# Optimization experiments

Measured on AMD Instinct MI355X. Metric: run time of the kernel, lower is better.

The kernel has to match this reference:

```python
import jax, jax.numpy as jnp
import numpy as np

N_TOKENS = 16384
DIM = 2048
HIDDEN = 1408
N_EXPERTS = 8


def setup_inputs() -> dict:
    key = jax.random.key(0)
    k_x, k_w1, k_w2, k_w3 = jax.random.split(key, 4)
    x = jax.random.normal(k_x, (N_TOKENS, DIM), dtype=jnp.float32)
    # trunc_normal(std=0.02) approximated by scaled normal
    w1 = jax.random.normal(k_w1, (N_EXPERTS, HIDDEN, DIM), dtype=jnp.float32) * 0.02
    w2 = jax.random.normal(k_w2, (N_EXPERTS, DIM, HIDDEN), dtype=jnp.float32) * 0.02
    w3 = jax.random.normal(k_w3, (N_EXPERTS, HIDDEN, DIM), dtype=jnp.float32) * 0.02
    # contiguous, even token split across experts (sums to N_TOKENS)
    num_tokens_per_expert = jnp.full((N_EXPERTS,), N_TOKENS // N_EXPERTS, dtype=jnp.int32)
    return {"x": x, "w1": w1, "w2": w2, "w3": w3,
            "num_tokens_per_expert": num_tokens_per_expert}


def reference(x, w1, w2, w3, num_tokens_per_expert):
    """Masked per-expert SwiGLU FFN (matches _run_experts_for_loop).

    x: [N, D] tokens sorted so expert e owns the contiguous slice
       [cumsum_shifted[e], cumsum[e]).
    """
    n_tokens = x.shape[0]
    n_experts = w1.shape[0]
    cumsum = jnp.cumsum(num_tokens_per_expert.astype(jnp.int32))
    cumsum_shifted = jnp.concatenate(
        [jnp.zeros((1,), dtype=cumsum.dtype), cumsum[:-1]])
    token_idx = jnp.arange(n_tokens)
    out = jnp.zeros_like(x)
    for e in range(n_experts):  # small fixed expert loop, unrolled under jit
        mask = ((token_idx >= cumsum_shifted[e]) & (token_idx < cumsum[e]))
        mask = mask.astype(x.dtype)[:, None]          # [N, 1]
        x_masked = x * mask                            # [N, D]
        h = jax.nn.silu(x_masked @ w1[e].T)            # [N, H]
        h = h * (x_masked @ w3[e].T)                   # [N, H]
        out = out + (h @ w2[e].T) * mask               # [N, D]
    return out
```

## Files before the change

### kernel.cpp

```cpp
#include <hip/hip_runtime.h>
#include <stdint.h>

#define NTOK 16384
#define DIM 2048
#define HIDDEN 1408
#define NEXP 8
#define NPRIME 2816

typedef short short8 __attribute__((ext_vector_type(8)));
typedef float f32x4 __attribute__((ext_vector_type(4)));
typedef unsigned short u16;

__device__ __forceinline__ u16 f2bf(float f) {
    uint32_t u = __float_as_uint(f);
    return (u16)((u + 0x7fffu + ((u >> 16) & 1u)) >> 16);
}

__device__ __forceinline__ void gload16(const u16* g, u16* l) {
    __builtin_amdgcn_global_load_lds(
        (const __attribute__((address_space(1))) void*)g,
        (__attribute__((address_space(3))) void*)l,
        16, 0, 0);
}

__global__ __launch_bounds__(256) void cvt_kernel(const float* __restrict__ src,
                                                  u16* __restrict__ dst, long n) {
    long i0 = ((long)blockIdx.x * 256 + threadIdx.x) * 8;
    long stride = (long)gridDim.x * 256 * 8;
    for (long i = i0; i < n; i += stride) {
        float4 a = *(const float4*)(src + i);
        float4 b = *(const float4*)(src + i + 4);
        uint4 o;
        o.x = (uint32_t)f2bf(a.x) | ((uint32_t)f2bf(a.y) << 16);
        o.y = (uint32_t)f2bf(a.z) | ((uint32_t)f2bf(a.w) << 16);
        o.z = (uint32_t)f2bf(b.x) | ((uint32_t)f2bf(b.y) << 16);
        o.w = (uint32_t)f2bf(b.z) | ((uint32_t)f2bf(b.w) << 16);
        *(uint4*)(dst + i) = o;
    }
}

__global__ __launch_bounds__(256) void cvt13_kernel(const float* __restrict__ w1,
                                                    const float* __restrict__ w3,
                                                    u16* __restrict__ dst) {
    const int r  = blockIdx.x;
    const int e  = r / NPRIME;
    const int np = r - e * NPRIME;
    const int p  = np >> 5;
    const int s  = (np >> 4) & 1;
    const int c  = np & 15;
    const int hcol = p * 16 + c;
    const float* src = (s ? w3 : w1) + ((size_t)e * HIDDEN + hcol) * DIM;
    u16* d = dst + (size_t)r * DIM;
    const int i = threadIdx.x * 8;
    float4 a = *(const float4*)(src + i);
    float4 b = *(const float4*)(src + i + 4);
    uint4 o;
    o.x = (uint32_t)f2bf(a.x) | ((uint32_t)f2bf(a.y) << 16);
    o.y = (uint32_t)f2bf(a.z) | ((uint32_t)f2bf(a.w) << 16);
    o.z = (uint32_t)f2bf(b.x) | ((uint32_t)f2bf(b.y) << 16);
    o.w = (uint32_t)f2bf(b.z) | ((uint32_t)f2bf(b.w) << 16);
    *(uint4*)(d + i) = o;
}

__global__ __launch_bounds__(256) void ffn1_kernel(
    const u16* __restrict__ xb, const u16* __restrict__ wb13,
    const int* __restrict__ ntpe, u16* __restrict__ hb)
{
    __shared__ u16 As[128 * 64];
    __shared__ u16 Bs[128 * 64];

    const int e  = blockIdx.z;
    const int mt = blockIdx.x;
    const int nt = blockIdx.y;

    int base = 0;
    #pragma unroll
    for (int i = 0; i < NEXP; ++i) base += (i < e) ? ntpe[i] : 0;
    const int cnt = ntpe[e];
    if (mt * 128 >= cnt) return;

    const int tid  = threadIdx.x;
    const int lane = tid & 63;
    const int wid  = tid >> 6;
    const int wr   = wid >> 1;
    const int wc   = wid & 1;
    const int lq   = lane >> 4;
    const int lm   = lane & 15;

    const size_t m0 = (size_t)base + (size_t)mt * 128;
    const u16* Ag = xb   + m0 * DIM;
    const u16* Bg = wb13 + ((size_t)e * NPRIME + nt * 128) * DIM;

    f32x4 acc[4][4] = {};

    for (int k0 = 0; k0 < DIM; k0 += 64) {
        if (k0) __syncthreads();
        #pragma unroll
        for (int it = 0; it < 4; ++it) {
            int c   = it * 256 + tid;
            int row = c >> 3;
            int col = ((c & 7) ^ (row & 7)) * 8;
            size_t go = (size_t)row * DIM + k0 + col;
            gload16(Ag + go, &As[c * 8]);
            gload16(Bg + go, &Bs[c * 8]);
        }
        __syncthreads();

        #pragma unroll
        for (int kk = 0; kk < 2; ++kk) {
            const int gc = kk * 4 + lq;
            short8 af[4], bf[4];
            #pragma unroll
            for (int i = 0; i < 4; ++i) {
                int ar = wr * 64 + i * 16 + lm;
                af[i] = *(const short8*)&As[ar * 64 + ((gc ^ (ar & 7)) << 3)];
                int br = wc * 64 + i * 16 + lm;
                bf[i] = *(const short8*)&Bs[br * 64 + ((gc ^ (br & 7)) << 3)];
            }
            #pragma unroll
            for (int i = 0; i < 4; ++i)
                #pragma unroll
                for (int j = 0; j < 4; ++j)
                    acc[i][j] = __builtin_amdgcn_mfma_f32_16x16x32_bf16(af[i], bf[j], acc[i][j], 0, 0, 0);
        }
    }

    #pragma unroll
    for (int i = 0; i < 4; ++i)
        #pragma unroll
        for (int jp = 0; jp < 4; jp += 2) {
            const int p = nt * 4 + wc * 2 + (jp >> 1);
            #pragma unroll
            for (int r = 0; r < 4; ++r) {
                int mrow = mt * 128 + wr * 64 + i * 16 + lq * 4 + r;
                if (mrow < cnt) {
                    float v1 = acc[i][jp][r];
                    float v3 = acc[i][jp + 1][r];
                    float h = (v1 / (1.f + __expf(-v1))) * v3;
                    hb[((size_t)base + mrow) * HIDDEN + p * 16 + lm] = f2bf(h);
                }
            }
        }
}

__global__ __launch_bounds__(256) void ffn2_kernel(
    const u16* __restrict__ hb, const u16* __restrict__ w2b,
    const int* __restrict__ ntpe, float* __restrict__ out)
{
    __shared__ u16 As[128 * 64];
    __shared__ u16 Bs[128 * 64];

    const int e  = blockIdx.z;
    const int mt = blockIdx.x;
    const int nt = blockIdx.y;

    int base = 0;
    #pragma unroll
    for (int i = 0; i < NEXP; ++i) base += (i < e) ? ntpe[i] : 0;
    const int cnt = ntpe[e];
    if (mt * 128 >= cnt) return;

    const int tid  = threadIdx.x;
    const int lane = tid & 63;
    const int wid  = tid >> 6;
    const int wr   = wid >> 1;
    const int wc   = wid & 1;
    const int lq   = lane >> 4;
    const int lm   = lane & 15;

    const size_t m0 = (size_t)base + (size_t)mt * 128;
    const int    n0 = nt * 128;
    const u16* Ag = hb  + m0 * HIDDEN;
    const u16* Bg = w2b + ((size_t)e * DIM + n0) * HIDDEN;

    f32x4 acc[4][4] = {};

    for (int k0 = 0; k0 < HIDDEN; k0 += 64) {
        if (k0) __syncthreads();
        #pragma unroll
        for (int it = 0; it < 4; ++it) {
            int c   = it * 256 + tid;
            int row = c >> 3;
            int col = ((c & 7) ^ (row & 7)) * 8;
            size_t go = (size_t)row * HIDDEN + k0 + col;
            gload16(Ag + go, &As[c * 8]);
            gload16(Bg + go, &Bs[c * 8]);
        }
        __syncthreads();

        #pragma unroll
        for (int kk = 0; kk < 2; ++kk) {
            const int gc = kk * 4 + lq;
            short8 af[4], bf[4];
            #pragma unroll
            for (int i = 0; i < 4; ++i) {
                int ar = wr * 64 + i * 16 + lm;
                af[i] = *(const short8*)&As[ar * 64 + ((gc ^ (ar & 7)) << 3)];
                int br = wc * 64 + i * 16 + lm;
                bf[i] = *(const short8*)&Bs[br * 64 + ((gc ^ (br & 7)) << 3)];
            }
            #pragma unroll
            for (int i = 0; i < 4; ++i)
                #pragma unroll
                for (int j = 0; j < 4; ++j)
                    acc[i][j] = __builtin_amdgcn_mfma_f32_16x16x32_bf16(af[i], bf[j], acc[i][j], 0, 0, 0);
        }
    }

    #pragma unroll
    for (int i = 0; i < 4; ++i)
        #pragma unroll
        for (int j = 0; j < 4; ++j)
            #pragma unroll
            for (int r = 0; r < 4; ++r) {
                int mrow = mt * 128 + wr * 64 + i * 16 + lq * 4 + r;
                if (mrow < cnt)
                    out[((size_t)base + mrow) * DIM + (n0 + wc * 64 + j * 16 + lm)] = acc[i][j][r];
            }
}

extern "C" void kernel_launch(void* const* d_in, const int* in_sizes, int n_in,
                              void* d_out, int out_size, void* d_ws, size_t ws_size,
                              hipStream_t stream) {
    const float* x  = (const float*)d_in[0];
    const float* w1 = (const float*)d_in[1];
    const float* w2 = (const float*)d_in[2];
    const float* w3 = (const float*)d_in[3];
    const int* ntpe = (const int*)d_in[4];
    float* out = (float*)d_out;

    u16* xb   = (u16*)d_ws;
    u16* wb13 = xb   + (size_t)NTOK * DIM;
    u16* w2b  = wb13 + (size_t)NEXP * NPRIME * DIM;
    u16* hb   = w2b  + (size_t)NEXP * DIM * HIDDEN;

    cvt_kernel<<<2048, 256, 0, stream>>>(x,  xb,  (long)NTOK * DIM);
    cvt_kernel<<<2048, 256, 0, stream>>>(w2, w2b, (long)NEXP * DIM * HIDDEN);
    cvt13_kernel<<<NEXP * NPRIME, 256, 0, stream>>>(w1, w3, wb13);

    ffn1_kernel<<<dim3(16, 22, NEXP), 256, 0, stream>>>(xb, wb13, ntpe, hb);
    ffn2_kernel<<<dim3(16, 16, NEXP), 256, 0, stream>>>(hb, w2b, ntpe, out);
}
```

Baseline: 431.0 us.

## Triple-buffer GEMM mainloop with 256x128 tiles, 8 waves and XCD-aware block remap

Both FFN GEMMs now run 512-thread blocks on 256x128 output tiles. The K loop uses a three-stage LDS ring: the loads for tile t+2 are issued while tile t is computed, with explicit vmcnt waits and raw barriers instead of a sync-load-sync step per tile. MFMA sections run at raised wave priority, and the 1D grid is remapped so consecutive logical tiles spread across the XCDs. The aim is to hide global-to-LDS latency and cut redundant operand traffic, at the cost of about 147KB of LDS per block, which allows only one block per CU and relies on tight barrier and vmcnt accounting.

```diff
diff --git a/kernel.cpp b/kernel.cpp
--- a/kernel.cpp
+++ b/kernel.cpp
@@ -21,6 +21,25 @@
         (const __attribute__((address_space(1))) void*)g,
         (__attribute__((address_space(3))) void*)l,
         16, 0, 0);
+}
+
+__device__ __forceinline__ void stageA(const u16* Ag, size_t lda, int k2, u16* dst, int tid) {
+    #pragma unroll
+    for (int it = 0; it < 4; ++it) {
+        int c   = it * 512 + tid;
+        int row = c >> 3;
+        int sc  = ((c & 7) ^ (row & 7)) << 3;
+        gload16(Ag + (size_t)row * lda + k2 + sc, dst + c * 16 / 2);
+    }
+}
+__device__ __forceinline__ void stageB(const u16* Bg, size_t ldb, int k2, u16* dst, int tid) {
+    #pragma unroll
+    for (int it = 0; it < 2; ++it) {
+        int c   = it * 512 + tid;
+        int row = c >> 3;
+        int sc  = ((c & 7) ^ (row & 7)) << 3;
+        gload16(Bg + (size_t)row * ldb + k2 + sc, dst + c * 8);
+    }
 }
 
 __global__ __launch_bounds__(256) void cvt_kernel(const float* __restrict__ src,
@@ -62,68 +81,104 @@
     *(uint4*)(d + i) = o;
 }
 
-__global__ __launch_bounds__(256) void ffn1_kernel(
+
+#define GEMM_CORE(LD, NT, ACC_DECL)                                              \
+    const int tid  = threadIdx.x;                                                \
+    const int lane = tid & 63;                                                   \
+    const int wid  = tid >> 6;                                                   \
+    const int wr   = wid >> 1;                         \
+    const int wc   = wid & 1;                          \
+    const int lq   = lane >> 4;                                                  \
+    const int lm   = lane & 15;                                                  \
+    ACC_DECL;                                                                    \
+    stageA(Ag, LD, 0,  As[0], tid);  stageB(Bg, LD, 0,  Bs[0], tid);             \
+    stageA(Ag, LD, 64, As[1], tid);  stageB(Bg, LD, 64, Bs[1], tid);             \
+    asm volatile("s_waitcnt vmcnt(6)" ::: "memory");                             \
+    __builtin_amdgcn_s_barrier();                                                \
+    for (int t = 0; t < NT; ++t) {                                               \
+        const int p = t % 3, q = (t + 2) % 3;                                    \
+        const u16* Asp = As[p];                                                  \
+        const u16* Bsp = Bs[p];                                                  \
+        short8 af0[2][2], af1[2][2], bf[4][2];                                   \
+        _Pragma("unroll")                                                        \
+        for (int i = 0; i < 2; ++i)                                              \
+            _Pragma("unroll")                                                    \
+            for (int kk = 0; kk < 2; ++kk) {                                     \
+                int ar = wr * 64 + i * 16 + lm;                                  \
+                int gc = kk * 4 + lq;                                            \
+                af0[i][kk] = *(const short8*)&Asp[ar * 64 + ((gc ^ (ar & 7)) << 3)]; \
+            }                                                                    \
+        _Pragma("unroll")                                                        \
+        for (int j = 0; j < 4; ++j)                                              \
+            _Pragma("unroll")                                                    \
+            for (int kk = 0; kk < 2; ++kk) {                                     \
+                int br = wc * 64 + j * 16 + lm;                                  \
+                int gc = kk * 4 + lq;                                            \
+                bf[j][kk] = *(const short8*)&Bsp[br * 64 + ((gc ^ (br & 7)) << 3)]; \
+            }                                                                    \
+        if (t + 2 < NT) stageA(Ag, LD, (t + 2) * 64, As[q], tid);                \
+        __builtin_amdgcn_s_barrier();                                            \
+        __builtin_amdgcn_s_setprio(1);                                           \
+        _Pragma("unroll")                                                        \
+        for (int kk = 0; kk < 2; ++kk)                                           \
+            _Pragma("unroll")                                                    \
+            for (int i = 0; i < 2; ++i)                                          \
+                _Pragma("unroll")                                                \
+                for (int j = 0; j < 4; ++j)                                      \
+                    acc[i][j] = __builtin_amdgcn_mfma_f32_16x16x32_bf16(         \
+                        af0[i][kk], bf[j][kk], acc[i][j], 0, 0, 0);              \
+        __builtin_amdgcn_s_setprio(0);                                           \
+        __builtin_amdgcn_s_barrier();                                            \
+        _Pragma("unroll")                                                        \
+        for (int i = 0; i < 2; ++i)                                              \
+            _Pragma("unroll")                                                    \
+            for (int kk = 0; kk < 2; ++kk) {                                     \
+                int ar = wr * 64 + (i + 2) * 16 + lm;                            \
+                int gc = kk * 4 + lq;                                            \
+                af1[i][kk] = *(const short8*)&Asp[ar * 64 + ((gc ^ (ar & 7)) << 3)]; \
+            }                                                                    \
+        if (t + 2 < NT) stageB(Bg, LD, (t + 2) * 64, Bs[q], tid);                \
+        __builtin_amdgcn_s_barrier();                                            \
+        __builtin_amdgcn_s_setprio(1);                                           \
+        _Pragma("unroll")                                                        \
+        for (int kk = 0; kk < 2; ++kk)                                           \
+            _Pragma("unroll")                                                    \
+            for (int i = 0; i < 2; ++i)                                          \
+                _Pragma("unroll")                                                \
+                for (int j = 0; j < 4; ++j)                                      \
+                    acc[i + 2][j] = __builtin_amdgcn_mfma_f32_16x16x32_bf16(     \
+                        af1[i][kk], bf[j][kk], acc[i + 2][j], 0, 0, 0);          \
+        __builtin_amdgcn_s_setprio(0);                                           \
+        if (t + 2 < NT) { asm volatile("s_waitcnt vmcnt(6)" ::: "memory"); }     \
+        else            { asm volatile("s_waitcnt vmcnt(0)" ::: "memory"); }     \
+        __builtin_amdgcn_s_barrier();                                            \
+    }
+
+__global__ __launch_bounds__(512, 1) void ffn1_kernel(
     const u16* __restrict__ xb, const u16* __restrict__ wb13,
     const int* __restrict__ ntpe, u16* __restrict__ hb)
 {
-    __shared__ u16 As[128 * 64];
-    __shared__ u16 Bs[128 * 64];
-
-    const int e  = blockIdx.z;
-    const int mt = blockIdx.x;
-    const int nt = blockIdx.y;
+    __shared__ u16 As[3][256 * 64];
+    __shared__ u16 Bs[3][128 * 64];
+
+    const int nwg = 8 * 22 * NEXP;
+    int logical = (blockIdx.x & 7) * (nwg >> 3) + (blockIdx.x >> 3);
+    const int mt = logical & 7;
+    int rest = logical >> 3;
+    const int nt = rest % 22;
+    const int e  = rest / 22;
 
     int base = 0;
     #pragma unroll
     for (int i = 0; i < NEXP; ++i) base += (i < e) ? ntpe[i] : 0;
     const int cnt = ntpe[e];
-    if (mt * 128 >= cnt) return;
-
-    const int tid  = threadIdx.x;
-    const int lane = tid & 63;
-    const int wid  = tid >> 6;
-    const int wr   = wid >> 1;
-    const int wc   = wid & 1;
-    const int lq   = lane >> 4;
-    const int lm   = lane & 15;
-
-    const size_t m0 = (size_t)base + (size_t)mt * 128;
+    if (mt * 256 >= cnt) return;
+
+    const size_t m0 = (size_t)base + (size_t)mt * 256;
     const u16* Ag = xb   + m0 * DIM;
     const u16* Bg = wb13 + ((size_t)e * NPRIME + nt * 128) * DIM;
 
-    f32x4 acc[4][4] = {};
-
-    for (int k0 = 0; k0 < DIM; k0 += 64) {
-        if (k0) __syncthreads();
-        #pragma unroll
-        for (int it = 0; it < 4; ++it) {
-            int c   = it * 256 + tid;
-            int row = c >> 3;
-            int col = ((c & 7) ^ (row & 7)) * 8;
-            size_t go = (size_t)row * DIM + k0 + col;
-            gload16(Ag + go, &As[c * 8]);
-            gload16(Bg + go, &Bs[c * 8]);
-        }
-        __syncthreads();
-
-        #pragma unroll
-        for (int kk = 0; kk < 2; ++kk) {
-            const int gc = kk * 4 + lq;
-            short8 af[4], bf[4];
-            #pragma unroll
-            for (int i = 0; i < 4; ++i) {
-                int ar = wr * 64 + i * 16 + lm;
-                af[i] = *(const short8*)&As[ar * 64 + ((gc ^ (ar & 7)) << 3)];
-                int br = wc * 64 + i * 16 + lm;
-                bf[i] = *(const short8*)&Bs[br * 64 + ((gc ^ (br & 7)) << 3)];
-            }
-            #pragma unroll
-            for (int i = 0; i < 4; ++i)
-                #pragma unroll
-                for (int j = 0; j < 4; ++j)
-                    acc[i][j] = __builtin_amdgcn_mfma_f32_16x16x32_bf16(af[i], bf[j], acc[i][j], 0, 0, 0);
-        }
-    }
+    GEMM_CORE(DIM, 32, f32x4 acc[4][4] = {})
 
     #pragma unroll
     for (int i = 0; i < 4; ++i)
@@ -132,7 +187,7 @@
             const int p = nt * 4 + wc * 2 + (jp >> 1);
             #pragma unroll
             for (int r = 0; r < 4; ++r) {
-                int mrow = mt * 128 + wr * 64 + i * 16 + lq * 4 + r;
+                int mrow = mt * 256 + wr * 64 + i * 16 + lq * 4 + r;
                 if (mrow < cnt) {
                     float v1 = acc[i][jp][r];
                     float v3 = acc[i][jp + 1][r];
@@ -143,69 +198,31 @@
         }
 }
 
-__global__ __launch_bounds__(256) void ffn2_kernel(
+__global__ __launch_bounds__(512, 1) void ffn2_kernel(
     const u16* __restrict__ hb, const u16* __restrict__ w2b,
     const int* __restrict__ ntpe, float* __restrict__ out)
 {
-    __shared__ u16 As[128 * 64];
-    __shared__ u16 Bs[128 * 64];
-
-    const int e  = blockIdx.z;
-    const int mt = blockIdx.x;
-    const int nt = blockIdx.y;
+    __shared__ u16 As[3][256 * 64];
+    __shared__ u16 Bs[3][128 * 64];
+
+    const int nwg = 8 * 16 * NEXP;
+    int logical = (blockIdx.x & 7) * (nwg >> 3) + (blockIdx.x >> 3);
+    const int mt = logical & 7;
+    int rest = logical >> 3;
+    const int nt = rest % 16;
+    const int e  = rest / 16;
 
     int base = 0;
     #pragma unroll
     for (int i = 0; i < NEXP; ++i) base += (i < e) ? ntpe[i] : 0;
     const int cnt = ntpe[e];
-    if (mt * 128 >= cnt) return;
-
-    const int tid  = threadIdx.x;
-    const int lane = tid & 63;
-    const int wid  = tid >> 6;
-    const int wr   = wid >> 1;
-    const int wc   = wid & 1;
-    const int lq   = lane >> 4;
-    const int lm   = lane & 15;
-
-    const size_t m0 = (size_t)base + (size_t)mt * 128;
-    const int    n0 = nt * 128;
+    if (mt * 256 >= cnt) return;
+
+    const size_t m0 = (size_t)base + (size_t)mt * 256;
     const u16* Ag = hb  + m0 * HIDDEN;
-    const u16* Bg = w2b + ((size_t)e * DIM + n0) * HIDDEN;
-
-    f32x4 acc[4][4] = {};
-
-    for (int k0 = 0; k0 < HIDDEN; k0 += 64) {
-        if (k0) __syncthreads();
-        #pragma unroll
-        for (int it = 0; it < 4; ++it) {
-            int c   = it * 256 + tid;
-            int row = c >> 3;
-            int col = ((c & 7) ^ (row & 7)) * 8;
-            size_t go = (size_t)row * HIDDEN + k0 + col;
-            gload16(Ag + go, &As[c * 8]);
-            gload16(Bg + go, &Bs[c * 8]);
-        }
-        __syncthreads();
-
-        #pragma unroll
-        for (int kk = 0; kk < 2; ++kk) {
-            const int gc = kk * 4 + lq;
-            short8 af[4], bf[4];
-            #pragma unroll
-            for (int i = 0; i < 4; ++i) {
-                int ar = wr * 64 + i * 16 + lm;
-                af[i] = *(const short8*)&As[ar * 64 + ((gc ^ (ar & 7)) << 3)];
-                int br = wc * 64 + i * 16 + lm;
-                bf[i] = *(const short8*)&Bs[br * 64 + ((gc ^ (br & 7)) << 3)];
-            }
-            #pragma unroll
-            for (int i = 0; i < 4; ++i)
-                #pragma unroll
-                for (int j = 0; j < 4; ++j)
-                    acc[i][j] = __builtin_amdgcn_mfma_f32_16x16x32_bf16(af[i], bf[j], acc[i][j], 0, 0, 0);
-        }
-    }
+    const u16* Bg = w2b + ((size_t)e * DIM + nt * 128) * HIDDEN;
+
+    GEMM_CORE(HIDDEN, 22, f32x4 acc[4][4] = {})
 
     #pragma unroll
     for (int i = 0; i < 4; ++i)
@@ -213,9 +230,9 @@
         for (int j = 0; j < 4; ++j)
             #pragma unroll
             for (int r = 0; r < 4; ++r) {
-                int mrow = mt * 128 + wr * 64 + i * 16 + lq * 4 + r;
+                int mrow = mt * 256 + wr * 64 + i * 16 + lq * 4 + r;
                 if (mrow < cnt)
-                    out[((size_t)base + mrow) * DIM + (n0 + wc * 64 + j * 16 + lm)] = acc[i][j][r];
+                    out[((size_t)base + mrow) * DIM + (nt * 128 + wc * 64 + j * 16 + lm)] = acc[i][j][r];
             }
 }
 
@@ -238,6 +255,6 @@
     cvt_kernel<<<2048, 256, 0, stream>>>(w2, w2b, (long)NEXP * DIM * HIDDEN);
     cvt13_kernel<<<NEXP * NPRIME, 256, 0, stream>>>(w1, w3, wb13);
 
-    ffn1_kernel<<<dim3(16, 22, NEXP), 256, 0, stream>>>(xb, wb13, ntpe, hb);
-    ffn2_kernel<<<dim3(16, 16, NEXP), 256, 0, stream>>>(hb, w2b, ntpe, out);
-}
+    ffn1_kernel<<<8 * 22 * NEXP, 512, 0, stream>>>(xb, wb13, ntpe, hb);
+    ffn2_kernel<<<8 * 16 * NEXP, 512, 0, stream>>>(hb, w2b, ntpe, out);
+}
```

After: 508.6 us. 18.0% more time.
